# Kernel optimization log

Measured on AMD Instinct MI355X. Metric: run time of the kernel, lower is better.

## Reference

```python
import jax, jax.numpy as jnp
import numpy as np

B = 2048
F = 267          # frame_size
L = 32           # latent_size
H = 256          # hidden_size (hard-coded in module)
E = 8            # num_experts
G = 64           # gate hidden size (hard-coded)
IN0 = L + F      # decoder layer0 input (latent + frame*cond_frames)
IN1 = L + H      # decoder inter input
OUT = F          # num_future_predictions * frame_size


def _lin_init(key, out_dim, in_dim):
    # kaiming-uniform-like scale
    bound = float(np.sqrt(1.0 / in_dim))
    return jax.random.uniform(key, (out_dim, in_dim), jnp.float32, -bound, bound)


def setup_inputs() -> dict:
    key = jax.random.key(0)
    ks = jax.random.split(key, 24)
    d = {}
    d["x"] = jax.random.normal(ks[0], (B, F), jnp.float32)
    d["c"] = jax.random.normal(ks[1], (B, F), jnp.float32)
    # encoder
    d["fc1_w"] = _lin_init(ks[2], H, 2 * F); d["fc1_b"] = jnp.zeros((H,), jnp.float32)
    d["fc2_w"] = _lin_init(ks[3], H, F + H); d["fc2_b"] = jnp.zeros((H,), jnp.float32)
    d["mu_w"] = _lin_init(ks[4], L, F + H);  d["mu_b"] = jnp.zeros((L,), jnp.float32)
    d["lv_w"] = _lin_init(ks[5], L, F + H);  d["lv_b"] = jnp.zeros((L,), jnp.float32)
    # gate
    d["g0_w"] = _lin_init(ks[6], G, IN0); d["g0_b"] = jnp.zeros((G,), jnp.float32)
    d["g1_w"] = _lin_init(ks[7], G, G);   d["g1_b"] = jnp.zeros((G,), jnp.float32)
    d["g2_w"] = _lin_init(ks[8], E, G);   d["g2_b"] = jnp.zeros((E,), jnp.float32)
    # expert weights [E, in, out], biases [E, out], bias filled 0.01 as in module
    d["w0"] = jax.random.uniform(ks[9], (E, IN0, H), jnp.float32, -1, 1) * np.sqrt(1.0 / IN0)
    d["b0"] = jnp.full((E, H), 0.01, jnp.float32)
    d["w1"] = jax.random.uniform(ks[10], (E, IN1, H), jnp.float32, -1, 1) * np.sqrt(1.0 / IN1)
    d["b1"] = jnp.full((E, H), 0.01, jnp.float32)
    d["w2"] = jax.random.uniform(ks[11], (E, IN1, OUT), jnp.float32, -1, 1) * np.sqrt(1.0 / IN1)
    d["b2"] = jnp.full((E, OUT), 0.01, jnp.float32)
    return d


def reference(x, c, fc1_w, fc1_b, fc2_w, fc2_b, mu_w, mu_b, lv_w, lv_b,
              g0_w, g0_b, g1_w, g1_b, g2_w, g2_b, w0, b0, w1, b1, w2, b2):
    elu = jax.nn.elu
    # ---- encoder ----
    h1 = elu(jnp.concatenate([x, c], axis=1) @ fc1_w.T + fc1_b)
    h2 = elu(jnp.concatenate([x, h1], axis=1) @ fc2_w.T + fc2_b)
    s = jnp.concatenate([x, h2], axis=1)
    mu = s @ mu_w.T + mu_b
    logvar = s @ lv_w.T + lv_b
    eps = jax.random.normal(jax.random.key(42), mu.shape, mu.dtype)
    z = mu + eps * jnp.exp(0.5 * logvar)
    # ---- mixed decoder ----
    g = elu(jnp.concatenate([z, c], axis=1) @ g0_w.T + g0_b)
    g = elu(g @ g1_w.T + g1_b)
    coeff = jax.nn.softmax(g @ g2_w.T + g2_b, axis=1)  # [B, E]
    layer_out = c
    for (W, bvec, act) in ((w0, b0, True), (w1, b1, True), (w2, b2, False)):
        inp = jnp.concatenate([z, layer_out], axis=1)          # [B, in]
        # per-expert GEMM then coefficient mixing (same math as per-sample
        # mixed-weight bmm: coeff @ flat_weight then baddbmm)
        out = jnp.einsum('be,bi,eio->bo', coeff, inp, W, optimize=True)
        out = out + coeff @ bvec                               # mixed bias
        layer_out = elu(out) if act else out
    return (layer_out, mu, logvar)
```

## Files before the change

kernel.cpp:

```cpp
#include <hip/hip_runtime.h>
#include <math.h>
#include <stdint.h>

#define DI __device__ __forceinline__

typedef __attribute__((ext_vector_type(8))) short bf16x8;
typedef __attribute__((ext_vector_type(4))) float f32x4;
typedef __attribute__((ext_vector_type(4))) int i32x4;

DI float elu_f(float v) { return v > 0.f ? v : expm1f(v); }

DI unsigned short f2bf(float f) {
  uint32_t u = __float_as_uint(f);
  return (unsigned short)((u + 0x7FFFu + ((u >> 16) & 1u)) >> 16);
}

DI void threefry2x32(uint32_t k0, uint32_t k1, uint32_t& x0, uint32_t& x1) {
  uint32_t ks0 = k0, ks1 = k1, ks2 = k0 ^ k1 ^ 0x1BD11BDAu;
  x0 += ks0; x1 += ks1;
#define TFR(r) { x0 += x1; x1 = (x1 << r) | (x1 >> (32 - r)); x1 ^= x0; }
  TFR(13) TFR(15) TFR(26) TFR(6)   x0 += ks1; x1 += ks2 + 1u;
  TFR(17) TFR(29) TFR(16) TFR(24)  x0 += ks2; x1 += ks0 + 2u;
  TFR(13) TFR(15) TFR(26) TFR(6)   x0 += ks0; x1 += ks1 + 3u;
  TFR(17) TFR(29) TFR(16) TFR(24)  x0 += ks1; x1 += ks2 + 4u;
  TFR(13) TFR(15) TFR(26) TFR(6)   x0 += ks2; x1 += ks0 + 5u;
#undef TFR
}

DI float erfinv_f(float x) {
  float w = -logf((1.0f - x) * (1.0f + x));
  float p;
  if (w < 5.0f) {
    w -= 2.5f;
    p = 2.81022636e-08f;
    p = fmaf(p, w, 3.43273939e-07f);
    p = fmaf(p, w, -3.5233877e-06f);
    p = fmaf(p, w, -4.39150654e-06f);
    p = fmaf(p, w, 0.00021858087f);
    p = fmaf(p, w, -0.00125372503f);
    p = fmaf(p, w, -0.00417768164f);
    p = fmaf(p, w, 0.246640727f);
    p = fmaf(p, w, 1.50140941f);
  } else {
    w = sqrtf(w) - 3.0f;
    p = -0.000200214257f;
    p = fmaf(p, w, 0.000100950558f);
    p = fmaf(p, w, 0.00134934322f);
    p = fmaf(p, w, -0.00367342844f);
    p = fmaf(p, w, 0.00573950773f);
    p = fmaf(p, w, -0.0076224613f);
    p = fmaf(p, w, 0.00943887047f);
    p = fmaf(p, w, 1.00167406f);
    p = fmaf(p, w, 2.83297682f);
  }
  return p * x;
}

struct MegaArgs {
  const float *x, *c;
  const float *fc1w, *fc1b, *fc2w, *fc2b, *muw, *mub, *lvw, *lvb;
  const float *g0w, *g0b, *g1w, *g1b, *g2w, *g2b;
  const float *w0, *b0, *w1, *b1, *w2, *b2;
  unsigned short *Ax, *Axh, *Axh2, *A0, *A1, *A2;
  unsigned short *fc1t, *fc2t, *mlvt, *g0t, *g1t, *w0b, *w1b, *w2b;
  float *cf, *outY, *outMu, *outLv;
};

template <int KT, int NE, int D, bool ELU, bool OUTF32, bool AREG>
__global__ __launch_bounds__(256, 1)
void pipe_gemm(const unsigned short* __restrict__ A,
               const unsigned short* __restrict__ Wt, int N,
               const float* __restrict__ bias,
               const float* __restrict__ cfp,
               unsigned short* __restrict__ Cb, int ldcb, int cb_off,
               float* __restrict__ Cf) {
  constexpr int Kp = KT * 32, LKA = Kp + 8, CPR = Kp / 8;
  constexpr int TT = NE * KT;
  __shared__ unsigned short As[32 * LKA];
  __shared__ float bias_s[NE * 64];
  __shared__ float cfs[256];
  const int tid = threadIdx.x, lane = tid & 63, wid = tid >> 6;
  const int q = lane >> 4, l16 = lane & 15;
  const int m0 = blockIdx.x * 32, n0 = blockIdx.y * 64;
  const int cl = wid * 16 + l16;
  const int gc = n0 + cl;
  const int wrow = (gc < N) ? gc : (N - 1);

  const unsigned short* wlane = Wt + (size_t)wrow * Kp + q * 8;

  bf16x8 ring[D];
#pragma unroll
  for (int g = 0; g < D; g++) {
    if (g < TT) {
      int e = g / KT, c = g % KT;
      ring[g] = *(const bf16x8*)(wlane + (size_t)e * N * Kp + c * 32);
    }
  }
  for (int idx = tid; idx < 32 * CPR; idx += 256) {
    int row = idx / CPR, ch = idx % CPR;
    *(i32x4*)(As + row * LKA + ch * 8) =
        *(const i32x4*)(A + (size_t)(m0 + row) * Kp + ch * 8);
  }
  for (int idx = tid; idx < NE * 64; idx += 256) {
    int e = idx >> 6, col = idx & 63;
    bias_s[idx] = (n0 + col < N) ? bias[(size_t)e * N + n0 + col] : 0.f;
  }
  if (NE > 1) cfs[tid] = cfp[(size_t)(m0 + (tid >> 3)) * 8 + (tid & 7)];
  __syncthreads();

  bf16x8 areg[AREG ? 2 * KT : 1];
  if (AREG) {
#pragma unroll
    for (int c = 0; c < KT; c++)
#pragma unroll
      for (int mi = 0; mi < 2; mi++)
        areg[c * 2 + mi] = *(const bf16x8*)(As + (mi * 16 + l16) * LKA + c * 32 + q * 8);
  }

  f32x4 acc[2] = {{0, 0, 0, 0}, {0, 0, 0, 0}};
  f32x4 accF[2] = {{0, 0, 0, 0}, {0, 0, 0, 0}};
#pragma unroll
  for (int g = 0; g < TT; g++) {
    const int e = g / KT, c = g % KT;
    bf16x8 bv = ring[g % D];
#pragma unroll
    for (int mi = 0; mi < 2; mi++) {
      bf16x8 av = AREG ? areg[c * 2 + mi]
                       : *(const bf16x8*)(As + (mi * 16 + l16) * LKA + c * 32 + q * 8);
      acc[mi] = __builtin_amdgcn_mfma_f32_16x16x32_bf16(av, bv, acc[mi], 0, 0, 0);
    }
    if (g + D < TT) {
      int e2 = (g + D) / KT, c2 = (g + D) % KT;
      ring[g % D] = *(const bf16x8*)(wlane + (size_t)e2 * N * Kp + c2 * 32);
    }
    if (NE > 1 && c == KT - 1) {
      float bv2 = bias_s[e * 64 + cl];
#pragma unroll
      for (int mi = 0; mi < 2; mi++)
#pragma unroll
        for (int r = 0; r < 4; r++) {
          float ce = cfs[(mi * 16 + q * 4 + r) * 8 + e];
          accF[mi][r] += ce * (acc[mi][r] + bv2);
          acc[mi][r] = 0.f;
        }
    }
  }

  if (gc < N) {
#pragma unroll
    for (int mi = 0; mi < 2; mi++)
#pragma unroll
      for (int r = 0; r < 4; r++) {
        int row = m0 + mi * 16 + q * 4 + r;
        float v = (NE > 1) ? accF[mi][r] : (acc[mi][r] + bias_s[cl]);
        if (ELU) v = elu_f(v);
        if (OUTF32) Cf[(size_t)row * 267 + gc] = v;
        else Cb[(size_t)row * ldcb + cb_off + gc] = f2bf(v);
      }
  }
}

__global__ __launch_bounds__(256) void k_prep(MegaArgs a) {
  __shared__ __align__(16) unsigned short T[64][72];
  const int bb = blockIdx.x, tid = threadIdx.x;
  if (bb < 512) {
    for (int rr = 0; rr < 4; rr++) {
      int b = bb * 4 + rr;
      const float* xr = a.x + (size_t)b * 267;
      const float* cr = a.c + (size_t)b * 267;
      unsigned short* axr = a.Ax + (size_t)b * 544;
      for (int k = tid; k < 544; k += 256) {
        float v = (k < 267) ? xr[k] : ((k < 534) ? cr[k - 267] : 0.f);
        axr[k] = f2bf(v);
      }
      unsigned short* ahr = a.Axh + (size_t)b * 544;
      unsigned short* ah2 = a.Axh2 + (size_t)b * 544;
      for (int k = tid; k < 267; k += 256) { unsigned short v = f2bf(xr[k]); ahr[k] = v; ah2[k] = v; }
      for (int k = 523 + tid; k < 544; k += 256) { ahr[k] = 0; ah2[k] = 0; }
      unsigned short* a0r = a.A0 + (size_t)b * 320;
      for (int k = tid; k < 288; k += 256)
        a0r[32 + k] = (k < 267) ? f2bf(cr[k]) : (unsigned short)0;
    }
  } else if (bb < 1152) {
    int r = bb - 512;
    const float* src; unsigned short* dst; int Ks, Kp2;
    if (r < 256)      { src = a.fc1w + (size_t)r * 534; dst = a.fc1t + (size_t)r * 544; Ks = 534; Kp2 = 544; }
    else if (r < 512) { int n = r - 256; src = a.fc2w + (size_t)n * 523; dst = a.fc2t + (size_t)n * 544; Ks = 523; Kp2 = 544; }
    else if (r < 576) { int n = r - 512; src = (n < 32) ? (a.muw + (size_t)n * 523) : (a.lvw + (size_t)(n - 32) * 523);
                        dst = a.mlvt + (size_t)n * 544; Ks = 523; Kp2 = 544; }
    else              { int n = r - 576; src = a.g0w + (size_t)n * 299; dst = a.g0t + (size_t)n * 320; Ks = 299; Kp2 = 320; }
    for (int k = tid; k < Kp2; k += 256) dst[k] = (k < Ks) ? f2bf(src[k]) : (unsigned short)0;
  } else if (bb == 1152) {
    for (int k = tid; k < 4096; k += 256) a.g1t[k] = f2bf(a.g1w[k]);
  } else {
    int t = bb - 1153;
    const float* W; unsigned short* D; int K, N2, Kp2, ldW, e, kt, nt;
    if (t < 160)      { e = t / 20;  int lt = t % 20;  kt = lt / 4; nt = lt % 4; W = a.w0; D = a.w0b; K = 299; N2 = 256; Kp2 = 320; ldW = 256; }
    else if (t < 320) { int u = t - 160; e = u / 20; int lt = u % 20; kt = lt / 4; nt = lt % 4; W = a.w1; D = a.w1b; K = 288; N2 = 256; Kp2 = 288; ldW = 256; }
    else              { int u = t - 320; e = u / 25; int lt = u % 25; kt = lt / 5; nt = lt % 5; W = a.w2; D = a.w2b; K = 288; N2 = 267; Kp2 = 288; ldW = 267; }
    const int k0 = kt * 64, n0 = nt * 64;
    const float* We = W + (size_t)e * K * ldW;
    const int jj = tid & 63, ii0 = tid >> 6;
#pragma unroll
    for (int p = 0; p < 16; p++) {
      int i = ii0 + p * 4;
      int gk = k0 + i, gn = n0 + jj;
      float v = (gk < K && gn < N2) ? We[(size_t)gk * ldW + gn] : 0.f;
      T[jj][i] = f2bf(v);
    }
    __syncthreads();
    int j = tid >> 2, chb = tid & 3;
    int gn = n0 + j;
    if (gn < N2) {
      unsigned short* drow = D + ((size_t)e * N2 + gn) * Kp2 + k0;
#pragma unroll
      for (int s = 0; s < 2; s++) {
        int ch = chb + s * 4;
        if (k0 + ch * 8 < Kp2) {
          i32x4 v = *(i32x4*)(&T[j][ch * 8]);
          *(i32x4*)(drow + ch * 8) = v;
        }
      }
    }
  }
}

__global__ __launch_bounds__(256, 1) void k_mulv_gate(MegaArgs a) {
  __shared__ __align__(16) unsigned char SM[64640];
  unsigned short* As  = (unsigned short*)SM;
  unsigned short* A0p = (unsigned short*)(SM + 35328);
  float* mlvS = (float*)(SM + 56320);
  unsigned short* gaB = (unsigned short*)SM;
  unsigned short* g1B = (unsigned short*)(SM + 4608);
  float* g2wT = (float*)(SM + 13824);
  float* lg   = (float*)(SM + 15872);
  float* gB   = (float*)(SM + 16896);

  const int tid = threadIdx.x, lane = tid & 63, wid = tid >> 6;
  const int q = lane >> 4, l16 = lane & 15;
  const int m0 = blockIdx.x * 32;
  const int cl = wid * 16 + l16;

  const unsigned short* wlA = a.mlvt + (size_t)cl * 544 + q * 8;
  bf16x8 ring[8];
#pragma unroll
  for (int g = 0; g < 8; g++) ring[g] = *(const bf16x8*)(wlA + g * 32);
  for (int idx = tid; idx < 32 * 68; idx += 256) {
    int row = idx / 68, ch = idx % 68;
    *(i32x4*)(As + row * 552 + ch * 8) =
        *(const i32x4*)(a.Axh2 + (size_t)(m0 + row) * 544 + ch * 8);
  }
  for (int idx = tid; idx < 32 * 36; idx += 256) {
    int row = idx / 36, ch = 4 + idx % 36;
    *(i32x4*)(A0p + row * 328 + ch * 8) =
        *(const i32x4*)(a.A0 + (size_t)(m0 + row) * 320 + ch * 8);
  }
  __syncthreads();
  f32x4 acc[2] = {{0, 0, 0, 0}, {0, 0, 0, 0}};
#pragma unroll
  for (int g = 0; g < 17; g++) {
    bf16x8 bv = ring[g % 8];
#pragma unroll
    for (int mi = 0; mi < 2; mi++) {
      bf16x8 av = *(const bf16x8*)(As + (mi * 16 + l16) * 552 + g * 32 + q * 8);
      acc[mi] = __builtin_amdgcn_mfma_f32_16x16x32_bf16(av, bv, acc[mi], 0, 0, 0);
    }
    if (g + 8 < 17) ring[g % 8] = *(const bf16x8*)(wlA + (g + 8) * 32);
  }
#pragma unroll
  for (int mi = 0; mi < 2; mi++)
#pragma unroll
    for (int r = 0; r < 4; r++)
      mlvS[(mi * 16 + q * 4 + r) * 65 + cl] = acc[mi][r];
  __syncthreads();

  {
    const int m = tid >> 3, j0 = (tid & 7) * 4, R = m0 + m;
#pragma unroll
    for (int jj = 0; jj < 4; jj++) {
      int j = j0 + jj;
      float mu = mlvS[m * 65 + j] + a.mub[j];
      float lvv = mlvS[m * 65 + j + 32] + a.lvb[j];
      uint32_t x0 = 0u, x1 = (uint32_t)(R * 32 + j);
      threefry2x32(0u, 42u, x0, x1);
      uint32_t bits = x0 ^ x1;
      float f = __uint_as_float((bits >> 9) | 0x3F800000u) - 1.0f;
      const float lo = -0.99999994039535522461f;
      float u = fmaf(f, 2.0f, lo);
      u = fmaxf(u, lo);
      float eps = 1.41421356237f * erfinv_f(u);
      float z = fmaf(eps, expf(0.5f * lvv), mu);
      a.outMu[(size_t)R * 32 + j] = mu;
      a.outLv[(size_t)R * 32 + j] = lvv;
      unsigned short zb = f2bf(z);
      A0p[m * 328 + j] = zb;
      a.A0[(size_t)R * 320 + j] = zb;
      a.A1[(size_t)R * 288 + j] = zb;
      a.A2[(size_t)R * 288 + j] = zb;
    }
  }
  for (int idx = tid; idx < 512; idx += 256) {
    int row = idx >> 3, ch = idx & 7;
    *(i32x4*)(g1B + row * 72 + ch * 8) = *(const i32x4*)(a.g1t + (size_t)row * 64 + ch * 8);
  }
  for (int idx = tid; idx < 512; idx += 256)
    g2wT[(idx & 63) * 8 + (idx >> 6)] = a.g2w[idx];
  __syncthreads();

  const unsigned short* wlC = a.g0t + (size_t)cl * 320 + q * 8;
  bf16x8 ring2[8];
#pragma unroll
  for (int g = 0; g < 8; g++) ring2[g] = *(const bf16x8*)(wlC + g * 32);
  f32x4 accC[2] = {{0, 0, 0, 0}, {0, 0, 0, 0}};
#pragma unroll
  for (int g = 0; g < 10; g++) {
    bf16x8 bv = ring2[g % 8];
#pragma unroll
    for (int mi = 0; mi < 2; mi++) {
      bf16x8 av = *(const bf16x8*)(A0p + (mi * 16 + l16) * 328 + g * 32 + q * 8);
      accC[mi] = __builtin_amdgcn_mfma_f32_16x16x32_bf16(av, bv, accC[mi], 0, 0, 0);
    }
    if (g + 8 < 10) ring2[g % 8] = *(const bf16x8*)(wlC + (g + 8) * 32);
  }
  {
    float bc = a.g0b[cl];
#pragma unroll
    for (int mi = 0; mi < 2; mi++)
#pragma unroll
      for (int r = 0; r < 4; r++)
        gaB[(mi * 16 + q * 4 + r) * 72 + cl] = f2bf(elu_f(accC[mi][r] + bc));
  }
  __syncthreads();

  f32x4 acc2[2] = {{0, 0, 0, 0}, {0, 0, 0, 0}};
#pragma unroll
  for (int tau = 0; tau < 2; tau++) {
    bf16x8 bv = *(const bf16x8*)(g1B + (size_t)cl * 72 + tau * 32 + q * 8);
#pragma unroll
    for (int mi = 0; mi < 2; mi++) {
      bf16x8 av = *(const bf16x8*)(gaB + (mi * 16 + l16) * 72 + tau * 32 + q * 8);
      acc2[mi] = __builtin_amdgcn_mfma_f32_16x16x32_bf16(av, bv, acc2[mi], 0, 0, 0);
    }
  }
  {
    float bc = a.g1b[cl];
#pragma unroll
    for (int mi = 0; mi < 2; mi++)
#pragma unroll
      for (int r = 0; r < 4; r++)
        gB[(mi * 16 + q * 4 + r) * 65 + cl] = elu_f(acc2[mi][r] + bc);
  }
  __syncthreads();

  {
    int r = tid >> 3, e = tid & 7;
    float d = a.g2b[e];
#pragma unroll 8
    for (int k = 0; k < 64; k++) d = fmaf(gB[r * 65 + k], g2wT[k * 8 + e], d);
    lg[r * 8 + e] = d;
  }
  __syncthreads();
  if (tid < 32) {
    float mx = lg[tid * 8];
#pragma unroll
    for (int e2 = 1; e2 < 8; e2++) mx = fmaxf(mx, lg[tid * 8 + e2]);
    float s = 0.f, ex[8];
#pragma unroll
    for (int e2 = 0; e2 < 8; e2++) { ex[e2] = expf(lg[tid * 8 + e2] - mx); s += ex[e2]; }
    float inv = 1.f / s;
#pragma unroll
    for (int e2 = 0; e2 < 8; e2++) a.cf[(size_t)(m0 + tid) * 8 + e2] = ex[e2] * inv;
  }
}

extern "C" void kernel_launch(void* const* d_in, const int* in_sizes, int n_in,
                              void* d_out, int out_size, void* d_ws, size_t ws_size,
                              hipStream_t stream) {
  (void)in_sizes; (void)n_in; (void)out_size; (void)ws_size;
  float* out = (float*)d_out;
  float* ws = (float*)d_ws;

  MegaArgs a;
  a.x    = (const float*)d_in[0];
  a.c    = (const float*)d_in[1];
  a.fc1w = (const float*)d_in[2];  a.fc1b = (const float*)d_in[3];
  a.fc2w = (const float*)d_in[4];  a.fc2b = (const float*)d_in[5];
  a.muw  = (const float*)d_in[6];  a.mub  = (const float*)d_in[7];
  a.lvw  = (const float*)d_in[8];  a.lvb  = (const float*)d_in[9];
  a.g0w  = (const float*)d_in[10]; a.g0b  = (const float*)d_in[11];
  a.g1w  = (const float*)d_in[12]; a.g1b  = (const float*)d_in[13];
  a.g2w  = (const float*)d_in[14]; a.g2b  = (const float*)d_in[15];
  a.w0   = (const float*)d_in[16]; a.b0   = (const float*)d_in[17];
  a.w1   = (const float*)d_in[18]; a.b1   = (const float*)d_in[19];
  a.w2   = (const float*)d_in[20]; a.b2   = (const float*)d_in[21];

  a.outY  = out;
  a.outMu = out + 2048 * 267;
  a.outLv = a.outMu + 2048 * 32;

  a.Ax   = (unsigned short*)(ws);
  a.Axh  = (unsigned short*)(ws + 557056);
  a.Axh2 = (unsigned short*)(ws + 1114112);
  a.A0   = (unsigned short*)(ws + 1671168);
  a.A1   = (unsigned short*)(ws + 1998848);
  a.A2   = (unsigned short*)(ws + 2293760);
  a.fc1t = (unsigned short*)(ws + 2588672);
  a.fc2t = (unsigned short*)(ws + 2658304);
  a.mlvt = (unsigned short*)(ws + 2727936);
  a.g0t  = (unsigned short*)(ws + 2745344);
  a.g1t  = (unsigned short*)(ws + 2755584);
  a.w0b  = (unsigned short*)(ws + 2757632);
  a.w1b  = (unsigned short*)(ws + 3085312);
  a.w2b  = (unsigned short*)(ws + 3380224);
  a.cf   = ws + 3687808;

  dim3 blk(256);
  k_prep<<<1673, blk, 0, stream>>>(a);
  pipe_gemm<17, 1, 12, true, false, false><<<dim3(64, 4), blk, 0, stream>>>(
      a.Ax, a.fc1t, 256, a.fc1b, nullptr, a.Axh, 544, 267, nullptr);
  pipe_gemm<17, 1, 12, true, false, false><<<dim3(64, 4), blk, 0, stream>>>(
      a.Axh, a.fc2t, 256, a.fc2b, nullptr, a.Axh2, 544, 267, nullptr);
  k_mulv_gate<<<64, blk, 0, stream>>>(a);
  pipe_gemm<10, 8, 16, true, false, true><<<dim3(64, 4), blk, 0, stream>>>(
      a.A0, a.w0b, 256, a.b0, a.cf, a.A1, 288, 32, nullptr);
  pipe_gemm<9, 8, 16, true, false, true><<<dim3(64, 4), blk, 0, stream>>>(
      a.A1, a.w1b, 256, a.b1, a.cf, a.A2, 288, 32, nullptr);
  pipe_gemm<9, 8, 16, false, true, true><<<dim3(64, 5), blk, 0, stream>>>(
      a.A2, a.w2b, 267, a.b2, a.cf, nullptr, 0, 0, a.outY);
}
```

Measured before the change: 198.8 us.

## Shrink GEMM tiles to 32x16 per block and split mulv/gate across more blocks

Replaces the 256-thread, 32x64-tile GEMM with a 128-thread, 32x16-tile variant. Each wave now loads its own A rows straight from global memory into registers, so the shared-memory staging of A is gone. This gives four times as many blocks (1024 instead of 256), so more of the device's CUs get work on this small batch. The mu/logvar+gate kernel is also halved to 16 rows per block with 128 blocks, and the gate weight loads are moved earlier. The cost is that each weight column tile is read by more blocks, so redundant weight and A traffic through L2 rises and per-wave MFMA reuse is lower.

```diff
diff --git a/kernel.cpp b/kernel.cpp
--- a/kernel.cpp
+++ b/kernel.cpp
@@ -66,27 +66,24 @@
   float *cf, *outY, *outMu, *outLv;
 };
 
-template <int KT, int NE, int D, bool ELU, bool OUTF32, bool AREG>
-__global__ __launch_bounds__(256, 1)
-void pipe_gemm(const unsigned short* __restrict__ A,
-               const unsigned short* __restrict__ Wt, int N,
-               const float* __restrict__ bias,
-               const float* __restrict__ cfp,
-               unsigned short* __restrict__ Cb, int ldcb, int cb_off,
-               float* __restrict__ Cf) {
-  constexpr int Kp = KT * 32, LKA = Kp + 8, CPR = Kp / 8;
-  constexpr int TT = NE * KT;
-  __shared__ unsigned short As[32 * LKA];
-  __shared__ float bias_s[NE * 64];
-  __shared__ float cfs[256];
+template <int KT, int NE, int D, bool ELU, bool OUTF32>
+__global__ __launch_bounds__(128, 2)
+void pipe16(const unsigned short* __restrict__ A,
+            const unsigned short* __restrict__ Wt, int N,
+            const float* __restrict__ bias,
+            const float* __restrict__ cfp,
+            unsigned short* __restrict__ Cb, int ldcb, int cb_off,
+            float* __restrict__ Cf) {
+  constexpr int Kp = KT * 32, TT = NE * KT;
+  __shared__ float bias_s[NE * 16];
+  __shared__ float cfs[(NE > 1) ? 256 : 1];
   const int tid = threadIdx.x, lane = tid & 63, wid = tid >> 6;
   const int q = lane >> 4, l16 = lane & 15;
-  const int m0 = blockIdx.x * 32, n0 = blockIdx.y * 64;
-  const int cl = wid * 16 + l16;
-  const int gc = n0 + cl;
+  const int m0 = blockIdx.x * 32, n0 = blockIdx.y * 16;
+  const int gc = n0 + l16;
   const int wrow = (gc < N) ? gc : (N - 1);
-
   const unsigned short* wlane = Wt + (size_t)wrow * Kp + q * 8;
+  const unsigned short* alane = A + (size_t)(m0 + wid * 16 + l16) * Kp + q * 8;
 
   bf16x8 ring[D];
 #pragma unroll
@@ -96,67 +93,51 @@
       ring[g] = *(const bf16x8*)(wlane + (size_t)e * N * Kp + c * 32);
     }
   }
-  for (int idx = tid; idx < 32 * CPR; idx += 256) {
-    int row = idx / CPR, ch = idx % CPR;
-    *(i32x4*)(As + row * LKA + ch * 8) =
-        *(const i32x4*)(A + (size_t)(m0 + row) * Kp + ch * 8);
-  }
-  for (int idx = tid; idx < NE * 64; idx += 256) {
-    int e = idx >> 6, col = idx & 63;
-    bias_s[idx] = (n0 + col < N) ? bias[(size_t)e * N + n0 + col] : 0.f;
-  }
-  if (NE > 1) cfs[tid] = cfp[(size_t)(m0 + (tid >> 3)) * 8 + (tid & 7)];
-  __syncthreads();
-
-  bf16x8 areg[AREG ? 2 * KT : 1];
-  if (AREG) {
-#pragma unroll
-    for (int c = 0; c < KT; c++)
-#pragma unroll
-      for (int mi = 0; mi < 2; mi++)
-        areg[c * 2 + mi] = *(const bf16x8*)(As + (mi * 16 + l16) * LKA + c * 32 + q * 8);
-  }
-
-  f32x4 acc[2] = {{0, 0, 0, 0}, {0, 0, 0, 0}};
-  f32x4 accF[2] = {{0, 0, 0, 0}, {0, 0, 0, 0}};
+  bf16x8 areg[KT];
+#pragma unroll
+  for (int c = 0; c < KT; c++) areg[c] = *(const bf16x8*)(alane + c * 32);
+
+  if (NE == 1) {
+    if (tid < 16) bias_s[tid] = (n0 + tid < N) ? bias[n0 + tid] : 0.f;
+  } else {
+    if (tid < NE * 16) {
+      int e = tid >> 4, col = tid & 15;
+      bias_s[tid] = (n0 + col < N) ? bias[(size_t)e * N + n0 + col] : 0.f;
+    }
+    for (int idx = tid; idx < 256; idx += 128)
+      cfs[idx] = cfp[(size_t)(m0 + (idx >> 3)) * 8 + (idx & 7)];
+  }
+  __syncthreads();
+
+  f32x4 acc = {0.f, 0.f, 0.f, 0.f}, accF = {0.f, 0.f, 0.f, 0.f};
 #pragma unroll
   for (int g = 0; g < TT; g++) {
     const int e = g / KT, c = g % KT;
-    bf16x8 bv = ring[g % D];
-#pragma unroll
-    for (int mi = 0; mi < 2; mi++) {
-      bf16x8 av = AREG ? areg[c * 2 + mi]
-                       : *(const bf16x8*)(As + (mi * 16 + l16) * LKA + c * 32 + q * 8);
-      acc[mi] = __builtin_amdgcn_mfma_f32_16x16x32_bf16(av, bv, acc[mi], 0, 0, 0);
-    }
+    acc = __builtin_amdgcn_mfma_f32_16x16x32_bf16(areg[c], ring[g % D], acc, 0, 0, 0);
     if (g + D < TT) {
       int e2 = (g + D) / KT, c2 = (g + D) % KT;
       ring[g % D] = *(const bf16x8*)(wlane + (size_t)e2 * N * Kp + c2 * 32);
     }
     if (NE > 1 && c == KT - 1) {
-      float bv2 = bias_s[e * 64 + cl];
-#pragma unroll
-      for (int mi = 0; mi < 2; mi++)
-#pragma unroll
-        for (int r = 0; r < 4; r++) {
-          float ce = cfs[(mi * 16 + q * 4 + r) * 8 + e];
-          accF[mi][r] += ce * (acc[mi][r] + bv2);
-          acc[mi][r] = 0.f;
-        }
+      float bv2 = bias_s[e * 16 + l16];
+#pragma unroll
+      for (int r = 0; r < 4; r++) {
+        float ce = cfs[(wid * 16 + q * 4 + r) * 8 + e];
+        accF[r] += ce * (acc[r] + bv2);
+        acc[r] = 0.f;
+      }
     }
   }
 
   if (gc < N) {
 #pragma unroll
-    for (int mi = 0; mi < 2; mi++)
-#pragma unroll
-      for (int r = 0; r < 4; r++) {
-        int row = m0 + mi * 16 + q * 4 + r;
-        float v = (NE > 1) ? accF[mi][r] : (acc[mi][r] + bias_s[cl]);
-        if (ELU) v = elu_f(v);
-        if (OUTF32) Cf[(size_t)row * 267 + gc] = v;
-        else Cb[(size_t)row * ldcb + cb_off + gc] = f2bf(v);
-      }
+    for (int r = 0; r < 4; r++) {
+      int row = m0 + wid * 16 + q * 4 + r;
+      float v = (NE > 1) ? accF[r] : (acc[r] + bias_s[l16]);
+      if (ELU) v = elu_f(v);
+      if (OUTF32) Cf[(size_t)row * 267 + gc] = v;
+      else Cb[(size_t)row * ldcb + cb_off + gc] = f2bf(v);
+    }
   }
 }
 
@@ -225,59 +206,53 @@
   }
 }
 
-__global__ __launch_bounds__(256, 1) void k_mulv_gate(MegaArgs a) {
-  __shared__ __align__(16) unsigned char SM[64640];
-  unsigned short* As  = (unsigned short*)SM;
-  unsigned short* A0p = (unsigned short*)(SM + 35328);
-  float* mlvS = (float*)(SM + 56320);
-  unsigned short* gaB = (unsigned short*)SM;
-  unsigned short* g1B = (unsigned short*)(SM + 4608);
-  float* g2wT = (float*)(SM + 13824);
-  float* lg   = (float*)(SM + 15872);
-  float* gB   = (float*)(SM + 16896);
-
+__global__ __launch_bounds__(256, 2) void k_mulv_gate(MegaArgs a) {
+  __shared__ float mlvS[16 * 65];
+  __shared__ __align__(16) unsigned short A0p[16 * 328];
+  __shared__ __align__(16) unsigned short gaB[16 * 72];
+  __shared__ __align__(16) unsigned short g1B[64 * 72];
+  __shared__ float g2wT[64 * 8];
+  __shared__ float gB[16 * 65];
+  __shared__ float lg[16 * 8];
   const int tid = threadIdx.x, lane = tid & 63, wid = tid >> 6;
   const int q = lane >> 4, l16 = lane & 15;
-  const int m0 = blockIdx.x * 32;
+  const int m0 = blockIdx.x * 16;
   const int cl = wid * 16 + l16;
 
+  const unsigned short* alane = a.Axh2 + (size_t)(m0 + l16) * 544 + q * 8;
   const unsigned short* wlA = a.mlvt + (size_t)cl * 544 + q * 8;
   bf16x8 ring[8];
 #pragma unroll
   for (int g = 0; g < 8; g++) ring[g] = *(const bf16x8*)(wlA + g * 32);
-  for (int idx = tid; idx < 32 * 68; idx += 256) {
-    int row = idx / 68, ch = idx % 68;
-    *(i32x4*)(As + row * 552 + ch * 8) =
-        *(const i32x4*)(a.Axh2 + (size_t)(m0 + row) * 544 + ch * 8);
-  }
-  for (int idx = tid; idx < 32 * 36; idx += 256) {
+  bf16x8 areg[17];
+#pragma unroll
+  for (int c = 0; c < 17; c++) areg[c] = *(const bf16x8*)(alane + c * 32);
+  f32x4 acc = {0.f, 0.f, 0.f, 0.f};
+#pragma unroll
+  for (int g = 0; g < 17; g++) {
+    acc = __builtin_amdgcn_mfma_f32_16x16x32_bf16(areg[g], ring[g % 8], acc, 0, 0, 0);
+    if (g + 8 < 17) ring[g % 8] = *(const bf16x8*)(wlA + (g + 8) * 32);
+  }
+#pragma unroll
+  for (int r = 0; r < 4; r++) mlvS[(q * 4 + r) * 65 + cl] = acc[r];
+  for (int idx = tid; idx < 576; idx += 256) {
     int row = idx / 36, ch = 4 + idx % 36;
     *(i32x4*)(A0p + row * 328 + ch * 8) =
         *(const i32x4*)(a.A0 + (size_t)(m0 + row) * 320 + ch * 8);
   }
-  __syncthreads();
-  f32x4 acc[2] = {{0, 0, 0, 0}, {0, 0, 0, 0}};
-#pragma unroll
-  for (int g = 0; g < 17; g++) {
-    bf16x8 bv = ring[g % 8];
-#pragma unroll
-    for (int mi = 0; mi < 2; mi++) {
-      bf16x8 av = *(const bf16x8*)(As + (mi * 16 + l16) * 552 + g * 32 + q * 8);
-      acc[mi] = __builtin_amdgcn_mfma_f32_16x16x32_bf16(av, bv, acc[mi], 0, 0, 0);
-    }
-    if (g + 8 < 17) ring[g % 8] = *(const bf16x8*)(wlA + (g + 8) * 32);
-  }
-#pragma unroll
-  for (int mi = 0; mi < 2; mi++)
-#pragma unroll
-    for (int r = 0; r < 4; r++)
-      mlvS[(mi * 16 + q * 4 + r) * 65 + cl] = acc[mi][r];
+  if (tid < 16) { i32x4 z4 = {0, 0, 0, 0}; *(i32x4*)(A0p + tid * 328 + 320) = z4; }
+  for (int idx = tid; idx < 512; idx += 256) {
+    int row = idx >> 3, ch = idx & 7;
+    *(i32x4*)(g1B + row * 72 + ch * 8) = *(const i32x4*)(a.g1t + (size_t)row * 64 + ch * 8);
+  }
+  for (int idx = tid; idx < 512; idx += 256)
+    g2wT[(idx & 63) * 8 + (idx >> 6)] = a.g2w[idx];
   __syncthreads();
 
   {
-    const int m = tid >> 3, j0 = (tid & 7) * 4, R = m0 + m;
-#pragma unroll
-    for (int jj = 0; jj < 4; jj++) {
+    const int m = tid >> 4, j0 = (tid & 15) * 2, R = m0 + m;
+#pragma unroll
+    for (int jj = 0; jj < 2; jj++) {
       int j = j0 + jj;
       float mu = mlvS[m * 65 + j] + a.mub[j];
       float lvv = mlvS[m * 65 + j + 32] + a.lvb[j];
@@ -299,60 +274,43 @@
       a.A2[(size_t)R * 288 + j] = zb;
     }
   }
-  for (int idx = tid; idx < 512; idx += 256) {
-    int row = idx >> 3, ch = idx & 7;
-    *(i32x4*)(g1B + row * 72 + ch * 8) = *(const i32x4*)(a.g1t + (size_t)row * 64 + ch * 8);
-  }
-  for (int idx = tid; idx < 512; idx += 256)
-    g2wT[(idx & 63) * 8 + (idx >> 6)] = a.g2w[idx];
   __syncthreads();
 
   const unsigned short* wlC = a.g0t + (size_t)cl * 320 + q * 8;
   bf16x8 ring2[8];
 #pragma unroll
   for (int g = 0; g < 8; g++) ring2[g] = *(const bf16x8*)(wlC + g * 32);
-  f32x4 accC[2] = {{0, 0, 0, 0}, {0, 0, 0, 0}};
+  f32x4 accC = {0.f, 0.f, 0.f, 0.f};
 #pragma unroll
   for (int g = 0; g < 10; g++) {
-    bf16x8 bv = ring2[g % 8];
-#pragma unroll
-    for (int mi = 0; mi < 2; mi++) {
-      bf16x8 av = *(const bf16x8*)(A0p + (mi * 16 + l16) * 328 + g * 32 + q * 8);
-      accC[mi] = __builtin_amdgcn_mfma_f32_16x16x32_bf16(av, bv, accC[mi], 0, 0, 0);
-    }
+    bf16x8 av = *(const bf16x8*)(A0p + l16 * 328 + g * 32 + q * 8);
+    accC = __builtin_amdgcn_mfma_f32_16x16x32_bf16(av, ring2[g % 8], accC, 0, 0, 0);
     if (g + 8 < 10) ring2[g % 8] = *(const bf16x8*)(wlC + (g + 8) * 32);
   }
   {
     float bc = a.g0b[cl];
 #pragma unroll
-    for (int mi = 0; mi < 2; mi++)
-#pragma unroll
-      for (int r = 0; r < 4; r++)
-        gaB[(mi * 16 + q * 4 + r) * 72 + cl] = f2bf(elu_f(accC[mi][r] + bc));
-  }
-  __syncthreads();
-
-  f32x4 acc2[2] = {{0, 0, 0, 0}, {0, 0, 0, 0}};
+    for (int r = 0; r < 4; r++)
+      gaB[(q * 4 + r) * 72 + cl] = f2bf(elu_f(accC[r] + bc));
+  }
+  __syncthreads();
+
+  f32x4 accD = {0.f, 0.f, 0.f, 0.f};
 #pragma unroll
   for (int tau = 0; tau < 2; tau++) {
-    bf16x8 bv = *(const bf16x8*)(g1B + (size_t)cl * 72 + tau * 32 + q * 8);
-#pragma unroll
-    for (int mi = 0; mi < 2; mi++) {
-      bf16x8 av = *(const bf16x8*)(gaB + (mi * 16 + l16) * 72 + tau * 32 + q * 8);
-      acc2[mi] = __builtin_amdgcn_mfma_f32_16x16x32_bf16(av, bv, acc2[mi], 0, 0, 0);
-    }
+    bf16x8 av = *(const bf16x8*)(gaB + l16 * 72 + tau * 32 + q * 8);
+    bf16x8 bv = *(const bf16x8*)(g1B + cl * 72 + tau * 32 + q * 8);
+    accD = __builtin_amdgcn_mfma_f32_16x16x32_bf16(av, bv, accD, 0, 0, 0);
   }
   {
     float bc = a.g1b[cl];
 #pragma unroll
-    for (int mi = 0; mi < 2; mi++)
-#pragma unroll
-      for (int r = 0; r < 4; r++)
-        gB[(mi * 16 + q * 4 + r) * 65 + cl] = elu_f(acc2[mi][r] + bc);
-  }
-  __syncthreads();
-
-  {
+    for (int r = 0; r < 4; r++)
+      gB[(q * 4 + r) * 65 + cl] = elu_f(accD[r] + bc);
+  }
+  __syncthreads();
+
+  if (tid < 128) {
     int r = tid >> 3, e = tid & 7;
     float d = a.g2b[e];
 #pragma unroll 8
@@ -360,7 +318,7 @@
     lg[r * 8 + e] = d;
   }
   __syncthreads();
-  if (tid < 32) {
+  if (tid < 16) {
     float mx = lg[tid * 8];
 #pragma unroll
     for (int e2 = 1; e2 < 8; e2++) mx = fmaxf(mx, lg[tid * 8 + e2]);
@@ -414,17 +372,17 @@
   a.w2b  = (unsigned short*)(ws + 3380224);
   a.cf   = ws + 3687808;
 
-  dim3 blk(256);
-  k_prep<<<1673, blk, 0, stream>>>(a);
-  pipe_gemm<17, 1, 12, true, false, false><<<dim3(64, 4), blk, 0, stream>>>(
+  dim3 blkP(256), blkG(128);
+  k_prep<<<1673, blkP, 0, stream>>>(a);
+  pipe16<17, 1, 12, true, false><<<dim3(64, 16), blkG, 0, stream>>>(
       a.Ax, a.fc1t, 256, a.fc1b, nullptr, a.Axh, 544, 267, nullptr);
-  pipe_gemm<17, 1, 12, true, false, false><<<dim3(64, 4), blk, 0, stream>>>(
+  pipe16<17, 1, 12, true, false><<<dim3(64, 16), blkG, 0, stream>>>(
       a.Axh, a.fc2t, 256, a.fc2b, nullptr, a.Axh2, 544, 267, nullptr);
-  k_mulv_gate<<<64, blk, 0, stream>>>(a);
-  pipe_gemm<10, 8, 16, true, false, true><<<dim3(64, 4), blk, 0, stream>>>(
+  k_mulv_gate<<<128, blkP, 0, stream>>>(a);
+  pipe16<10, 8, 16, true, false><<<dim3(64, 16), blkG, 0, stream>>>(
       a.A0, a.w0b, 256, a.b0, a.cf, a.A1, 288, 32, nullptr);
-  pipe_gemm<9, 8, 16, true, false, true><<<dim3(64, 4), blk, 0, stream>>>(
+  pipe16<9, 8, 16, true, false><<<dim3(64, 16), blkG, 0, stream>>>(
       a.A1, a.w1b, 256, a.b1, a.cf, a.A2, 288, 32, nullptr);
-  pipe_gemm<9, 8, 16, false, true, true><<<dim3(64, 5), blk, 0, stream>>>(
+  pipe16<9, 8, 16, false, true><<<dim3(64, 17), blkG, 0, stream>>>(
       a.A2, a.w2b, 267, a.b2, a.cf, nullptr, 0, 0, a.outY);
 }
```

Measured after the change: 182.8 us. 1.09x faster.
